# Optimization experiments

Measured on AMD Instinct MI355X. Metric: run time of the kernel, lower is better.

## Reference

```python
import jax, jax.numpy as jnp
import numpy as np

B, N, E = 128, 196, 2048   # batch, num_features (14x14), encoder_dim
D, A = 512, 512            # decoder_dim, attention_dim


def setup_inputs() -> dict:
    key = jax.random.key(0)
    ks = jax.random.split(key, 8)
    s_e = 1.0 / np.sqrt(E)
    s_d = 1.0 / np.sqrt(D)
    s_a = 1.0 / np.sqrt(A)
    return {
        "encoder_out": jax.random.normal(ks[0], (B, N, E), dtype=jnp.float32),
        "decoder_hidden": jax.random.normal(ks[1], (B, D), dtype=jnp.float32),
        "We": jax.random.uniform(ks[2], (E, A), jnp.float32, -s_e, s_e),
        "be": jax.random.uniform(ks[3], (A,), jnp.float32, -s_e, s_e),
        "Wd": jax.random.uniform(ks[4], (D, A), jnp.float32, -s_d, s_d),
        "bd": jax.random.uniform(ks[5], (A,), jnp.float32, -s_d, s_d),
        "Wf": jax.random.uniform(ks[6], (A, 1), jnp.float32, -s_a, s_a),
        "bf": jax.random.uniform(ks[7], (1,), jnp.float32, -s_a, s_a),
    }


def reference(encoder_out, decoder_hidden, We, be, Wd, bd, Wf, bf):
    # att1: [B,N,A] projection of encoder features
    att1 = jnp.einsum('bne,ea->bna', encoder_out, We) + be
    # att2: [B,A] projection of decoder state, broadcast over N
    att2 = decoder_hidden @ Wd + bd
    att = jnp.tanh(att1 + att2[:, None, :])          # [B,N,A]
    scores = jnp.einsum('bna,ao->bno', att, Wf) + bf  # [B,N,1]
    alpha = jax.nn.softmax(scores, axis=1)            # softmax over num_features
    context = jnp.sum(encoder_out * alpha, axis=1)    # [B,E]
    return (context, alpha)
```

## Files before the change

kernel.cpp:

```cpp
#include <hip/hip_runtime.h>
#include <hip/hip_bf16.h>
#include <stdint.h>

#define B_   128
#define N_   196
#define E_   2048
#define D_   512
#define A_   512
#define MTOT (B_ * N_)

typedef short  short8  __attribute__((ext_vector_type(8)));
typedef float  floatx4 __attribute__((ext_vector_type(4)));

__device__ __forceinline__ unsigned short f2bf(float f) {
    union { float f; uint32_t u; } v; v.f = f;
    uint32_t r = v.u + 0x7FFFu + ((v.u >> 16) & 1u);
    return (unsigned short)(r >> 16);
}

__device__ __forceinline__ uint32_t pkbf(float a, float b) {
    uint32_t ua = __float_as_uint(a) + 0x8000u;
    uint32_t ub = __float_as_uint(b) + 0x8000u;
    return __builtin_amdgcn_perm(ub, ua, 0x07060302u);
}

__global__ void transcvt_k(const float* __restrict__ We, unsigned short* __restrict__ WeT2) {
    const int t   = threadIdx.x;
    const int l15 = t & 15;
    const int q4  = (t >> 4) & 3;
    const int g   = t >> 6;
    const int tile = blockIdx.x;
    const int kk   = blockIdx.y * 4 + g;
    const int a  = tile * 16 + l15;
    const int e0 = kk * 32 + q4 * 8;
    union { unsigned short us[8]; short8 s; } pk;
#pragma unroll
    for (int j = 0; j < 8; ++j)
        pk.us[j] = f2bf(We[(size_t)(e0 + j) * A_ + a]);
    *(short8*)(WeT2 + (size_t)tile * 32768 + kk * 512 + q4 * 128 + l15 * 8) = pk.s;
}

__launch_bounds__(512)
__global__ void att2_k(const float* __restrict__ dh, const float* __restrict__ Wd,
                       const float* __restrict__ bd, const float* __restrict__ be,
                       float* __restrict__ att2p) {
    const int b = blockIdx.x, t = threadIdx.x;
    __shared__ float sdh[D_];
    sdh[t] = dh[b * D_ + t];
    __syncthreads();
    float acc = 0.f;
#pragma unroll 8
    for (int d = 0; d < D_; ++d) acc += sdh[d] * Wd[(size_t)d * A_ + t];
    att2p[(size_t)b * A_ + t] = acc + bd[t] + be[t];
}

__launch_bounds__(256, 3)
__global__ void score_gemm(const float* __restrict__ enc,
                           const unsigned short* __restrict__ WeT2,
                           const float* __restrict__ att2p,
                           const float* __restrict__ Wf,
                           float* __restrict__ scoresP) {
    __shared__ __align__(16) char sMem[2][8192];
    __shared__ float sPart[4][64];

    const int t   = threadIdx.x;
    const int w   = t >> 6;
    const int l   = t & 63;
    const int l15 = l & 15;
    const int q4  = l >> 4;
    const int row0 = blockIdx.y * 64;
    const int col0 = blockIdx.x * 256;

    floatx4 acc[4][4] = {};

    const float* aSrc[2];
    int aDst[2];
#pragma unroll
    for (int h = 0; h < 2; ++h) {
        aSrc[h] = enc + (size_t)(row0 + w * 16 + l15) * E_ + (4 * h + q4) * 4;
        aDst[h] = w * 2048 + h * 1024 + l * 16;
    }

    const int ctBase = (col0 >> 4) + w * 4;
    const unsigned short* pbB[4];
#pragma unroll
    for (int ni = 0; ni < 4; ++ni)
        pbB[ni] = WeT2 + (size_t)(ctBase + ni) * 32768 + l * 8;

    const int offAlo = (2 * q4) * 256 + l15 * 16;

#pragma unroll
    for (int h = 0; h < 2; ++h)
        __builtin_amdgcn_global_load_lds(
            (const __attribute__((address_space(1))) uint32_t*)(aSrc[h]),
            (__attribute__((address_space(3))) uint32_t*)(&sMem[0][0] + aDst[h]), 16, 0, 0);
    short8 Bcur[4], Bnxt[4];
#pragma unroll
    for (int ni = 0; ni < 4; ++ni) Bcur[ni] = *(const short8*)(pbB[ni]);
    __syncthreads();

    for (int kk = 0; kk < 64; ++kk) {
        if (kk < 63) {
#pragma unroll
            for (int h = 0; h < 2; ++h)
                __builtin_amdgcn_global_load_lds(
                    (const __attribute__((address_space(1))) uint32_t*)(aSrc[h] + (kk + 1) * 32),
                    (__attribute__((address_space(3))) uint32_t*)(&sMem[(kk + 1) & 1][0] + aDst[h]),
                    16, 0, 0);
        }
        const char* aBuf = &sMem[kk & 1][0];
        union { uint32_t u[4]; short8 s; } af[4];
#pragma unroll
        for (int mi = 0; mi < 4; ++mi) {
            float4 lo = *(const float4*)(aBuf + mi * 2048 + offAlo);
            float4 hi = *(const float4*)(aBuf + mi * 2048 + offAlo + 256);
            af[mi].u[0] = pkbf(lo.x, lo.y);
            af[mi].u[1] = pkbf(lo.z, lo.w);
            af[mi].u[2] = pkbf(hi.x, hi.y);
            af[mi].u[3] = pkbf(hi.z, hi.w);
        }
        if (kk < 63) {
#pragma unroll
            for (int ni = 0; ni < 4; ++ni)
                Bnxt[ni] = *(const short8*)(pbB[ni] + (kk + 1) * 512);
        }
#pragma unroll
        for (int mi = 0; mi < 4; ++mi) {
            acc[mi][0] = __builtin_amdgcn_mfma_f32_16x16x32_bf16(af[mi].s, Bcur[0], acc[mi][0], 0, 0, 0);
            acc[mi][1] = __builtin_amdgcn_mfma_f32_16x16x32_bf16(af[mi].s, Bcur[1], acc[mi][1], 0, 0, 0);
            acc[mi][2] = __builtin_amdgcn_mfma_f32_16x16x32_bf16(af[mi].s, Bcur[2], acc[mi][2], 0, 0, 0);
            acc[mi][3] = __builtin_amdgcn_mfma_f32_16x16x32_bf16(af[mi].s, Bcur[3], acc[mi][3], 0, 0, 0);
        }
#pragma unroll
        for (int ni = 0; ni < 4; ++ni) Bcur[ni] = Bnxt[ni];
        __syncthreads();
    }

    const int cbase = col0 + w * 64;
    float wfv[4];
#pragma unroll
    for (int ni = 0; ni < 4; ++ni) wfv[ni] = Wf[cbase + ni * 16 + l15];

#pragma unroll
    for (int mi = 0; mi < 4; ++mi) {
#pragma unroll
        for (int r = 0; r < 4; ++r) {
            const int m    = mi * 16 + q4 * 4 + r;
            const int grow = row0 + m;
            const int bb   = grow / N_;
            const float* a2 = att2p + (size_t)bb * A_ + cbase;
            float s = 0.f;
#pragma unroll
            for (int ni = 0; ni < 4; ++ni) {
                float v  = acc[mi][ni][r] + a2[ni * 16 + l15];
                float e  = __expf(2.f * v);
                float th = 1.f - 2.f / (e + 1.f);
                s += th * wfv[ni];
            }
            s += __shfl_xor(s, 1);
            s += __shfl_xor(s, 2);
            s += __shfl_xor(s, 4);
            s += __shfl_xor(s, 8);
            if (l15 == 0) sPart[w][m] = s;
        }
    }
    __syncthreads();
    if (t < 64) {
        float v = sPart[0][t] + sPart[1][t] + sPart[2][t] + sPart[3][t];
        scoresP[(size_t)blockIdx.x * MTOT + row0 + t] = v;
    }
}

__global__ void softmax_k(const float* __restrict__ sp, float* __restrict__ alpha) {
    const int b = blockIdx.x, t = threadIdx.x;
    const int w = t >> 6, l = t & 63;
    __shared__ float red[8];
    float v = -3.0e38f;
    if (t < N_) v = sp[b * N_ + t] + sp[MTOT + b * N_ + t];
    float m = v;
#pragma unroll
    for (int off = 32; off >= 1; off >>= 1) m = fmaxf(m, __shfl_xor(m, off));
    if (l == 0) red[w] = m;
    __syncthreads();
    m = fmaxf(fmaxf(red[0], red[1]), fmaxf(red[2], red[3]));
    float e = 0.f;
    if (t < N_) e = __expf(v - m);
    float s = e;
#pragma unroll
    for (int off = 32; off >= 1; off >>= 1) s += __shfl_xor(s, off);
    if (l == 0) red[4 + w] = s;
    __syncthreads();
    s = red[4] + red[5] + red[6] + red[7];
    if (t < N_) alpha[b * N_ + t] = e / s;
}

__launch_bounds__(256)
__global__ void context_k(const float* __restrict__ enc, const float* __restrict__ alpha,
                          float* __restrict__ ctx) {
    const int chunk = blockIdx.x, b = blockIdx.y;
    const int t = threadIdx.x, tn = t >> 6, tc = t & 63;
    __shared__ float  sAl[N_];
    __shared__ float4 sRed[256];
    if (t < N_) sAl[t] = alpha[b * N_ + t];
    __syncthreads();
    const float* base = enc + (size_t)b * N_ * E_ + chunk * 256 + tc * 4;
    float4 a = make_float4(0.f, 0.f, 0.f, 0.f);
#pragma unroll 7
    for (int n = tn; n < N_; n += 4) {
        float  al = sAl[n];
        float4 v  = *(const float4*)(base + (size_t)n * E_);
        a.x += al * v.x; a.y += al * v.y; a.z += al * v.z; a.w += al * v.w;
    }
    sRed[t] = a;
    __syncthreads();
    if (t < 64) {
        float4 r0 = sRed[t], r1 = sRed[t + 64], r2 = sRed[t + 128], r3 = sRed[t + 192];
        float4 o = make_float4(r0.x + r1.x + r2.x + r3.x, r0.y + r1.y + r2.y + r3.y,
                               r0.z + r1.z + r2.z + r3.z, r0.w + r1.w + r2.w + r3.w);
        *(float4*)(ctx + (size_t)b * E_ + chunk * 256 + t * 4) = o;
    }
}

extern "C" void kernel_launch(void* const* d_in, const int* in_sizes, int n_in,
                              void* d_out, int out_size, void* d_ws, size_t ws_size,
                              hipStream_t stream) {
    const float* enc = (const float*)d_in[0];
    const float* dh  = (const float*)d_in[1];
    const float* We  = (const float*)d_in[2];
    const float* be  = (const float*)d_in[3];
    const float* Wd  = (const float*)d_in[4];
    const float* bd  = (const float*)d_in[5];
    const float* Wf  = (const float*)d_in[6];

    float* out   = (float*)d_out;
    float* ctx   = out;
    float* alpha = out + B_ * E_;

    char* ws = (char*)d_ws;
    unsigned short* WeT2 = (unsigned short*)ws;
    float* att2p         = (float*)(ws + (2u << 20));
    float* scoresP       = (float*)(ws + (2u << 20) + (256u << 10));

    transcvt_k <<<dim3(32, 16),       256, 0, stream>>>(We, WeT2);
    att2_k     <<<dim3(B_),           512, 0, stream>>>(dh, Wd, bd, be, att2p);
    score_gemm <<<dim3(2, MTOT / 64), 256, 0, stream>>>(enc, WeT2, att2p, Wf, scoresP);
    softmax_k  <<<dim3(B_),           256, 0, stream>>>(scoresP, alpha);
    context_k  <<<dim3(E_ / 256, B_), 256, 0, stream>>>(enc, alpha, ctx);
}
```

Measured before the change: 484.4 us.

## Triple-buffer encoder tiles with partial vmcnt waits in score GEMM

Replaces the double-buffered LDS staging of encoder rows with a three-buffer ring that prefetches two k-steps ahead. The full __syncthreads is replaced by an s_waitcnt vmcnt(2) plus a raw barrier, so the most recent DMA can stay in flight across the barrier. The main loop is unrolled by three so buffer selection is static. This raises LDS use per block from 16KB to 24KB and depends on the vmcnt count being exactly right. An incorrect count could read stale data.

```diff
diff --git a/kernel.cpp b/kernel.cpp
--- a/kernel.cpp
+++ b/kernel.cpp
@@ -60,7 +60,7 @@
                            const float* __restrict__ att2p,
                            const float* __restrict__ Wf,
                            float* __restrict__ scoresP) {
-    __shared__ __align__(16) char sMem[2][8192];
+    __shared__ __align__(16) char sA0[8192], sA1[8192], sA2[8192];
     __shared__ float sPart[4][64];
 
     const int t   = threadIdx.x;
@@ -89,52 +89,67 @@
 
     const int offAlo = (2 * q4) * 256 + l15 * 16;
 
-#pragma unroll
-    for (int h = 0; h < 2; ++h)
-        __builtin_amdgcn_global_load_lds(
-            (const __attribute__((address_space(1))) uint32_t*)(aSrc[h]),
-            (__attribute__((address_space(3))) uint32_t*)(&sMem[0][0] + aDst[h]), 16, 0, 0);
+#define DMA_A(KK, BUF) do {                                                   \
+        _Pragma("unroll")                                                     \
+        for (int h = 0; h < 2; ++h)                                           \
+            __builtin_amdgcn_global_load_lds(                                 \
+                (const __attribute__((address_space(1))) uint32_t*)(aSrc[h] + (KK) * 32), \
+                (__attribute__((address_space(3))) uint32_t*)((BUF) + aDst[h]), 16, 0, 0); \
+    } while (0)
+
+#define LOAD_B(DST, KK) do {                                                  \
+        _Pragma("unroll")                                                     \
+        for (int ni = 0; ni < 4; ++ni)                                        \
+            DST[ni] = *(const short8*)(pbB[ni] + (KK) * 512);                 \
+    } while (0)
+
+#define BAR() do {                                                            \
+        asm volatile("s_waitcnt vmcnt(2)" ::: "memory");                      \
+        __builtin_amdgcn_s_barrier();                                         \
+    } while (0)
+
+#define STEP(KK, RB, WB, NOTLAST) do {                                        \
+        union { uint32_t u[4]; short8 s; } af[4];                             \
+        _Pragma("unroll")                                                     \
+        for (int mi = 0; mi < 4; ++mi) {                                      \
+            float4 lo = *(const float4*)((RB) + mi * 2048 + offAlo);          \
+            float4 hi = *(const float4*)((RB) + mi * 2048 + offAlo + 256);    \
+            af[mi].u[0] = pkbf(lo.x, lo.y);                                   \
+            af[mi].u[1] = pkbf(lo.z, lo.w);                                   \
+            af[mi].u[2] = pkbf(hi.x, hi.y);                                   \
+            af[mi].u[3] = pkbf(hi.z, hi.w);                                   \
+        }                                                                     \
+        if (NOTLAST) LOAD_B(Bnxt, (KK) + 1);                                  \
+        _Pragma("unroll")                                                     \
+        for (int mi = 0; mi < 4; ++mi) {                                      \
+            acc[mi][0] = __builtin_amdgcn_mfma_f32_16x16x32_bf16(af[mi].s, Bcur[0], acc[mi][0], 0, 0, 0); \
+            acc[mi][1] = __builtin_amdgcn_mfma_f32_16x16x32_bf16(af[mi].s, Bcur[1], acc[mi][1], 0, 0, 0); \
+            acc[mi][2] = __builtin_amdgcn_mfma_f32_16x16x32_bf16(af[mi].s, Bcur[2], acc[mi][2], 0, 0, 0); \
+            acc[mi][3] = __builtin_amdgcn_mfma_f32_16x16x32_bf16(af[mi].s, Bcur[3], acc[mi][3], 0, 0, 0); \
+        }                                                                     \
+        if ((KK) < 62) DMA_A((KK) + 2, (WB));                                 \
+        _Pragma("unroll")                                                     \
+        for (int ni = 0; ni < 4; ++ni) Bcur[ni] = Bnxt[ni];                   \
+        if (NOTLAST) BAR();                                                   \
+    } while (0)
+
     short8 Bcur[4], Bnxt[4];
-#pragma unroll
-    for (int ni = 0; ni < 4; ++ni) Bcur[ni] = *(const short8*)(pbB[ni]);
-    __syncthreads();
-
-    for (int kk = 0; kk < 64; ++kk) {
-        if (kk < 63) {
-#pragma unroll
-            for (int h = 0; h < 2; ++h)
-                __builtin_amdgcn_global_load_lds(
-                    (const __attribute__((address_space(1))) uint32_t*)(aSrc[h] + (kk + 1) * 32),
-                    (__attribute__((address_space(3))) uint32_t*)(&sMem[(kk + 1) & 1][0] + aDst[h]),
-                    16, 0, 0);
-        }
-        const char* aBuf = &sMem[kk & 1][0];
-        union { uint32_t u[4]; short8 s; } af[4];
-#pragma unroll
-        for (int mi = 0; mi < 4; ++mi) {
-            float4 lo = *(const float4*)(aBuf + mi * 2048 + offAlo);
-            float4 hi = *(const float4*)(aBuf + mi * 2048 + offAlo + 256);
-            af[mi].u[0] = pkbf(lo.x, lo.y);
-            af[mi].u[1] = pkbf(lo.z, lo.w);
-            af[mi].u[2] = pkbf(hi.x, hi.y);
-            af[mi].u[3] = pkbf(hi.z, hi.w);
-        }
-        if (kk < 63) {
-#pragma unroll
-            for (int ni = 0; ni < 4; ++ni)
-                Bnxt[ni] = *(const short8*)(pbB[ni] + (kk + 1) * 512);
-        }
-#pragma unroll
-        for (int mi = 0; mi < 4; ++mi) {
-            acc[mi][0] = __builtin_amdgcn_mfma_f32_16x16x32_bf16(af[mi].s, Bcur[0], acc[mi][0], 0, 0, 0);
-            acc[mi][1] = __builtin_amdgcn_mfma_f32_16x16x32_bf16(af[mi].s, Bcur[1], acc[mi][1], 0, 0, 0);
-            acc[mi][2] = __builtin_amdgcn_mfma_f32_16x16x32_bf16(af[mi].s, Bcur[2], acc[mi][2], 0, 0, 0);
-            acc[mi][3] = __builtin_amdgcn_mfma_f32_16x16x32_bf16(af[mi].s, Bcur[3], acc[mi][3], 0, 0, 0);
-        }
-#pragma unroll
-        for (int ni = 0; ni < 4; ++ni) Bcur[ni] = Bnxt[ni];
-        __syncthreads();
-    }
+    DMA_A(0, sA0);
+    LOAD_B(Bcur, 0);
+    DMA_A(1, sA1);
+    BAR();
+
+    for (int k3 = 0; k3 < 63; k3 += 3) {
+        STEP(k3 + 0, sA0, sA2, true);
+        STEP(k3 + 1, sA1, sA0, true);
+        STEP(k3 + 2, sA2, sA1, true);
+    }
+    STEP(63, sA0, sA1, false);
+
+#undef DMA_A
+#undef LOAD_B
+#undef BAR
+#undef STEP
 
     const int cbase = col0 + w * 64;
     float wfv[4];
```

Result: no change. 483.1 us (-0.3%).
